# Optimization experiments

Measured on AMD Instinct MI355X. Metric: run time of the kernel, lower is better.

The kernel has to match this reference:

```python
import jax, jax.numpy as jnp
import numpy as np

B, K, DIN, D, NH, HD, FF = 16384, 64, 49, 16, 2, 8, 32
EPS = 1e-5


def _ln(x, g, b):
    m = jnp.mean(x, axis=-1, keepdims=True)
    v = jnp.mean((x - m) ** 2, axis=-1, keepdims=True)
    return (x - m) / jnp.sqrt(v + EPS) * g + b


def setup_inputs() -> dict:
    key = jax.random.key(0)
    ks = jax.random.split(key, 20)
    s = 0.05
    return {
        "x": jax.random.normal(ks[0], (B, K, DIN), dtype=jnp.float32),
        # torch Linear layout: weight is [out, in]
        "proj_w": jax.random.normal(ks[1], (D, DIN), dtype=jnp.float32) * s,
        "proj_b": jax.random.normal(ks[2], (D,), dtype=jnp.float32) * s,
        "pos": jax.random.normal(ks[3], (1, K, D), dtype=jnp.float32) * s,
        "in_proj_w": jax.random.normal(ks[4], (3 * D, D), dtype=jnp.float32) * s,
        "in_proj_b": jax.random.normal(ks[5], (3 * D,), dtype=jnp.float32) * s,
        "out_w": jax.random.normal(ks[6], (D, D), dtype=jnp.float32) * s,
        "out_b": jax.random.normal(ks[7], (D,), dtype=jnp.float32) * s,
        "ln1_g": jnp.ones((D,), dtype=jnp.float32),
        "ln1_b": jnp.zeros((D,), dtype=jnp.float32),
        "lin1_w": jax.random.normal(ks[8], (FF, D), dtype=jnp.float32) * s,
        "lin1_b": jax.random.normal(ks[9], (FF,), dtype=jnp.float32) * s,
        "lin2_w": jax.random.normal(ks[10], (D, FF), dtype=jnp.float32) * s,
        "lin2_b": jax.random.normal(ks[11], (D,), dtype=jnp.float32) * s,
        "ln2_g": jnp.ones((D,), dtype=jnp.float32),
        "ln2_b": jnp.zeros((D,), dtype=jnp.float32),
        "head_w": jax.random.normal(ks[12], (1, D), dtype=jnp.float32) * s,
        "head_b": jax.random.normal(ks[13], (1,), dtype=jnp.float32) * s,
    }


def reference(x, proj_w, proj_b, pos, in_proj_w, in_proj_b, out_w, out_b,
              ln1_g, ln1_b, lin1_w, lin1_b, lin2_w, lin2_b, ln2_g, ln2_b,
              head_w, head_b):
    # input projection + learned positional embedding
    h = jnp.einsum("bki,di->bkd", x, proj_w) + proj_b + pos  # [B,K,D]

    # --- self-attention (torch MultiheadAttention, post-norm encoder layer) ---
    qkv = jnp.einsum("bkd,ed->bke", h, in_proj_w) + in_proj_b  # [B,K,3D]
    q, k, v = jnp.split(qkv, 3, axis=-1)
    q = q.reshape(B, K, NH, HD)
    k = k.reshape(B, K, NH, HD)
    v = v.reshape(B, K, NH, HD)
    scores = jnp.einsum("bqhd,bkhd->bhqk", q, k) / jnp.sqrt(jnp.float32(HD))
    attn = jax.nn.softmax(scores, axis=-1)
    ctx = jnp.einsum("bhqk,bkhd->bqhd", attn, v).reshape(B, K, D)
    attn_out = jnp.einsum("bkd,od->bko", ctx, out_w) + out_b
    h = _ln(h + attn_out, ln1_g, ln1_b)

    # --- FFN (relu), post-norm ---
    ff = jnp.einsum("bkd,fd->bkf", h, lin1_w) + lin1_b
    ff = jax.nn.relu(ff)
    ff = jnp.einsum("bkf,df->bkd", ff, lin2_w) + lin2_b
    h = _ln(h + ff, ln2_g, ln2_b)

    # mean pool over sequence, then scalar head
    pooled = h.mean(axis=1)  # [B,D]
    out = jnp.einsum("bd,od->bo", pooled, head_w) + head_b
    return out.squeeze(-1)  # [B]
```

## Files before the change

### kernel.cpp

```cpp
#include <hip/hip_runtime.h>


#define SCALE 0.510069729f

#define KRS   24
#define VTB   1536
#define VTS   72
#define PRB   2688
#define PRS   72
#define HRB   7296
#define HRS   40
#define RED   9856
#define SMTOT 9864

#define WS_HB   2304
#define WS_EP   3328

typedef __bf16 v8bf __attribute__((ext_vector_type(8)));
typedef float  v4f  __attribute__((ext_vector_type(4)));

#define LDS_ORDER() __asm__ volatile("" ::: "memory")

static __device__ __forceinline__ short f2bs(float f) {
    __bf16 h = (__bf16)f;
    return __builtin_bit_cast(short, h);
}
#define MFMA(a,b,c) __builtin_amdgcn_mfma_f32_16x16x32_bf16((a),(b),(c),0,0,0)

template<int IMM> static __device__ __forceinline__ float swz(float x) {
    return __builtin_bit_cast(float,
        __builtin_amdgcn_ds_swizzle(__builtin_bit_cast(int, x), IMM));
}

static __device__ __forceinline__ void red16(v4f& v) {
    #pragma unroll
    for (int r = 0; r < 4; ++r) v[r] += swz<0x041F>(v[r]);
    #pragma unroll
    for (int r = 0; r < 4; ++r) v[r] += swz<0x081F>(v[r]);
    #pragma unroll
    for (int r = 0; r < 4; ++r) v[r] += swz<0x101F>(v[r]);
    #pragma unroll
    for (int r = 0; r < 4; ++r) v[r] += swz<0x201F>(v[r]);
}

__global__ __launch_bounds__(64)
void tx_prep(const float* __restrict__ proj_w, const float* __restrict__ proj_b,
             const float* __restrict__ pos,
             const float* __restrict__ in_proj_w, const float* __restrict__ in_proj_b,
             const float* __restrict__ out_w, const float* __restrict__ out_b,
             const float* __restrict__ ln1_g, const float* __restrict__ ln1_b,
             const float* __restrict__ lin1_w, const float* __restrict__ lin1_b,
             const float* __restrict__ lin2_w, const float* __restrict__ lin2_b,
             const float* __restrict__ ln2_g, const float* __restrict__ ln2_b,
             const float* __restrict__ head_w, float* __restrict__ ws)
{
    const int lane = threadIdx.x, g = lane >> 4, c = lane & 15;
    v8bf* wf = (v8bf*)ws;
    v8bf F;
    #pragma unroll
    for (int j = 0; j < 8; ++j) F[j] = (__bf16)proj_w[c*49 + g*8 + j];
    wf[0*64 + lane] = F;
    #pragma unroll
    for (int j = 0; j < 8; ++j) { int k = 32 + g*8 + j; F[j] = (k < 49) ? (__bf16)proj_w[c*49 + k] : (__bf16)0.f; }
    wf[1*64 + lane] = F;
    #pragma unroll
    for (int nt = 0; nt < 3; ++nt) {
        #pragma unroll
        for (int j = 0; j < 8; ++j) { int k = g*8 + j; F[j] = (k < 16) ? (__bf16)in_proj_w[(nt*16 + c)*16 + k] : (__bf16)0.f; }
        wf[(2 + nt)*64 + lane] = F;
    }
    #pragma unroll
    for (int j = 0; j < 8; ++j) { int k = g*8 + j; F[j] = (k < 16) ? (__bf16)out_w[c*16 + k] : (__bf16)0.f; }
    wf[5*64 + lane] = F;
    #pragma unroll
    for (int nt = 0; nt < 2; ++nt) {
        #pragma unroll
        for (int j = 0; j < 8; ++j) { int k = g*8 + j; F[j] = (k < 16) ? (__bf16)lin1_w[(nt*16 + c)*16 + k] : (__bf16)0.f; }
        wf[(6 + nt)*64 + lane] = F;
    }
    #pragma unroll
    for (int j = 0; j < 8; ++j) F[j] = (__bf16)lin2_w[c*32 + g*8 + j];
    wf[8*64 + lane] = F;

    float* hb = ws + WS_HB;
    #pragma unroll
    for (int ww = 0; ww < 4; ++ww)
        #pragma unroll
        for (int r = 0; r < 4; ++r)
            hb[ww*256 + lane*4 + r] = proj_b[c] + pos[(ww*16 + g*4 + r)*16 + c];

    if (lane < 16) {
        float* ep = ws + WS_EP + lane*16;
        ep[0]  = in_proj_b[lane];
        ep[1]  = in_proj_b[16 + lane] * SCALE;
        ep[2]  = in_proj_b[32 + lane];
        ep[3]  = out_b[lane];
        ep[4]  = ln1_g[lane];
        ep[5]  = ln1_b[lane];
        ep[6]  = lin1_b[lane];
        ep[7]  = lin1_b[16 + lane];
        ep[8]  = lin2_b[lane];
        ep[9]  = ln2_g[lane];
        ep[10] = ln2_b[lane];
        ep[11] = head_w[lane];
        ep[12] = 0.f; ep[13] = 0.f; ep[14] = 0.f; ep[15] = 0.f;
    }
}

__global__ __launch_bounds__(256, 8)
void tx_main(const float* __restrict__ x, const float* __restrict__ ws,
             const float* __restrict__ head_b, float* __restrict__ out)
{
    __shared__ __align__(16) short sm[SMTOT];
    const int tid   = threadIdx.x;
    const int w     = tid >> 6;
    const int lane  = tid & 63;
    const int g     = lane >> 4;
    const int c     = lane & 15;
    const int b     = blockIdx.x;
    const int myrow = w*16 + c;
    const int tok0  = w*16 + g*4;
    const v8bf* wf  = (const v8bf*)ws;
    const float4* ep4 = (const float4*)(ws + WS_EP);
    float* smf = (float*)sm;

    v8bf zfrag;
    #pragma unroll
    for (int j = 0; j < 8; ++j) zfrag[j] = (__bf16)0.f;
    const v4f zacc = {0.f, 0.f, 0.f, 0.f};

    const float4* xb4 = (const float4*)(x + (size_t)b * 3136);
    float4* sf4 = (float4*)smf;
    #pragma unroll
    for (int i = 0; i < 3; ++i) sf4[tid + i*256] = xb4[tid + i*256];
    if (tid < 16)      sf4[768 + tid] = xb4[768 + tid];
    else if (tid < 32) smf[3136 + tid - 16] = 0.f;
    *(unsigned long long*)&sm[HRB + myrow*HRS + 16 + g*4] = 0ull;
    __syncthreads();

    v4f hC;
    {
        const float* xr = smf + myrow*49 + g*8;
        v8bf a0, a1;
        #pragma unroll
        for (int j = 0; j < 8; ++j) a0[j] = (__bf16)xr[j];
        #pragma unroll
        for (int j = 0; j < 8; ++j) a1[j] = (__bf16)xr[32 + j];
        v8bf Bp0 = wf[0*64 + lane], Bp1 = wf[1*64 + lane];
        hC = MFMA(a0, Bp0, zacc);
        hC = MFMA(a1, Bp1, hC);
        v4f hb = ((const v4f*)(ws + WS_HB))[w*64 + lane];
        #pragma unroll
        for (int r = 0; r < 4; ++r) hC[r] += hb[r];
        #pragma unroll
        for (int r = 0; r < 4; ++r) sm[HRB + (tok0 + r)*HRS + c] = f2bs(hC[r]);
    }
    __syncthreads();

    {
        v8bf Bq0 = wf[2*64 + lane], Bq1 = wf[3*64 + lane], Bq2 = wf[4*64 + lane];
        v8bf a = *(const v8bf*)&sm[HRB + myrow*HRS + g*8];
        v4f qC = MFMA(a, Bq0, zacc);
        v4f kC = MFMA(a, Bq1, zacc);
        v4f vC = MFMA(a, Bq2, zacc);
        float4 e0 = ep4[c*4];
        #pragma unroll
        for (int r = 0; r < 4; ++r) {
            int tok = tok0 + r;
            sm[HRB + tok*HRS + c] = f2bs(qC[r] + e0.x);
            sm[tok*KRS + c]       = f2bs(fmaf(kC[r], SCALE, e0.y));
            sm[VTB + c*VTS + tok] = f2bs(vC[r] + e0.z);
        }
    }
    __syncthreads();

    v4f ctxC0, ctxC1;
    {
        v8bf aq = *(const v8bf*)&sm[HRB + myrow*HRS + g*8];
        const int ch  = c >> 3;
        const int pwb = PRB + tok0*PRS + (c & 7);
        const int prd = PRB + myrow*PRS + ((g ^ ((myrow >> 2) & 3)) << 3);
        #pragma unroll
        for (int hh = 0; hh < 2; ++hh) {
            v4f sC[4];
            #pragma unroll
            for (int tj = 0; tj < 4; ++tj) {
                v8bf bk = zfrag;
                if (g == hh) bk = *(const v8bf*)&sm[(tj*16 + c)*KRS + g*8];
                sC[tj] = MFMA(aq, bk, zacc);
            }
            #pragma unroll
            for (int tj = 0; tj < 4; ++tj) {
                int po = pwb + (((tj*2 + ch) ^ g) << 3);
                #pragma unroll
                for (int r = 0; r < 4; ++r)
                    sm[po + r*PRS] = f2bs(__builtin_amdgcn_exp2f(sC[tj][r]));
            }
            v8bf bv0 = zfrag, bv1 = zfrag;
            bool act  = (hh == 0) ? (c < 8) : (c >= 8);
            int  onec = (hh == 0) ? 8 : 7;
            if (act) {
                bv0 = *(const v8bf*)&sm[VTB + c*VTS + g*8];
                bv1 = *(const v8bf*)&sm[VTB + c*VTS + 32 + g*8];
            } else if (c == onec) {
                #pragma unroll
                for (int j = 0; j < 8; ++j) { bv0[j] = (__bf16)1.f; bv1[j] = (__bf16)1.f; }
            }
            LDS_ORDER();
            v4f acc = zacc;
            acc = MFMA(*(const v8bf*)&sm[prd],      bv0, acc);
            acc = MFMA(*(const v8bf*)&sm[prd + 32], bv1, acc);
            if (hh) ctxC1 = acc; else ctxC0 = acc;
            LDS_ORDER();
        }
    }

    {
        #pragma unroll
        for (int r = 0; r < 4; ++r) {
            float l0 = swz<0x110>(ctxC0[r]);
            float l1 = swz<0x0F0>(ctxC1[r]);
            float num = (c < 8) ? ctxC0[r] : ctxC1[r];
            float den = (c < 8) ? l0 : l1;
            sm[HRB + (tok0 + r)*HRS + c] = f2bs(num * __builtin_amdgcn_rcpf(den));
        }
    }
    LDS_ORDER();

    v4f hln;
    {
        v8bf Bo = wf[5*64 + lane];
        v8bf a = *(const v8bf*)&sm[HRB + myrow*HRS + g*8];
        v4f oC = MFMA(a, Bo, zacc);
        float4 e0 = ep4[c*4];
        float4 e1 = ep4[c*4 + 1];
        v4f hn, s, q;
        #pragma unroll
        for (int r = 0; r < 4; ++r) { hn[r] = hC[r] + oC[r] + e0.w; s[r] = hn[r]; q[r] = hn[r]*hn[r]; }
        red16(s);
        red16(q);
        #pragma unroll
        for (int r = 0; r < 4; ++r) {
            float mean = s[r]*0.0625f;
            float var  = fmaf(q[r], 0.0625f, -mean*mean);
            float is = __builtin_amdgcn_rsqf(var + 1e-5f);
            hln[r] = (hn[r] - mean)*is*e1.x + e1.y;
            sm[HRB + (tok0 + r)*HRS + c] = f2bs(hln[r]);
        }
    }
    LDS_ORDER();

    v4f o2;
    {
        v8bf Bl10 = wf[6*64 + lane], Bl11 = wf[7*64 + lane], Bl2 = wf[8*64 + lane];
        v8bf a = *(const v8bf*)&sm[HRB + myrow*HRS + g*8];
        v4f f0 = MFMA(a, Bl10, zacc);
        v4f f1 = MFMA(a, Bl11, zacc);
        float4 e1 = ep4[c*4 + 1];
        #pragma unroll
        for (int r = 0; r < 4; ++r) {
            int tok = tok0 + r;
            sm[HRB + tok*HRS + c]      = f2bs(fmaxf(f0[r] + e1.z, 0.f));
            sm[HRB + tok*HRS + 16 + c] = f2bs(fmaxf(f1[r] + e1.w, 0.f));
        }
        LDS_ORDER();
        v8bf a2 = *(const v8bf*)&sm[HRB + myrow*HRS + g*8];
        o2 = MFMA(a2, Bl2, zacc);
    }

    float part = 0.f;
    {
        float4 e2 = ep4[c*4 + 2];
        v4f hn, s, q;
        #pragma unroll
        for (int r = 0; r < 4; ++r) { hn[r] = hln[r] + o2[r] + e2.x; s[r] = hn[r]; q[r] = hn[r]*hn[r]; }
        red16(s);
        red16(q);
        #pragma unroll
        for (int r = 0; r < 4; ++r) {
            float mean = s[r]*0.0625f;
            float var  = fmaf(q[r], 0.0625f, -mean*mean);
            float is = __builtin_amdgcn_rsqf(var + 1e-5f);
            float h3 = (hn[r] - mean)*is*e2.y + e2.z;
            part = fmaf(h3, e2.w, part);
        }
    }
    part += swz<0x041F>(part);
    part += swz<0x081F>(part);
    part += swz<0x101F>(part);
    part += swz<0x201F>(part);
    part += swz<0x401F>(part);
    part += __shfl_xor(part, 32, 64);
    float* fred = (float*)&sm[RED];
    if (lane == 0) fred[w] = part;
    __syncthreads();
    if (tid == 0)
        out[b] = (fred[0] + fred[1] + fred[2] + fred[3]) * (1.f/64.f) + head_b[0];
}

extern "C" void kernel_launch(void* const* d_in, const int* in_sizes, int n_in,
                              void* d_out, int out_size, void* d_ws, size_t ws_size,
                              hipStream_t stream) {
    const float* x         = (const float*)d_in[0];
    const float* proj_w    = (const float*)d_in[1];
    const float* proj_b    = (const float*)d_in[2];
    const float* pos       = (const float*)d_in[3];
    const float* in_proj_w = (const float*)d_in[4];
    const float* in_proj_b = (const float*)d_in[5];
    const float* out_w     = (const float*)d_in[6];
    const float* out_b     = (const float*)d_in[7];
    const float* ln1_g     = (const float*)d_in[8];
    const float* ln1_b     = (const float*)d_in[9];
    const float* lin1_w    = (const float*)d_in[10];
    const float* lin1_b    = (const float*)d_in[11];
    const float* lin2_w    = (const float*)d_in[12];
    const float* lin2_b    = (const float*)d_in[13];
    const float* ln2_g     = (const float*)d_in[14];
    const float* ln2_b     = (const float*)d_in[15];
    const float* head_w    = (const float*)d_in[16];
    const float* head_b    = (const float*)d_in[17];
    float* ws = (float*)d_ws;

    tx_prep<<<1, 64, 0, stream>>>(proj_w, proj_b, pos, in_proj_w, in_proj_b,
                                  out_w, out_b, ln1_g, ln1_b, lin1_w, lin1_b,
                                  lin2_w, lin2_b, ln2_g, ln2_b, head_w, ws);
    tx_main<<<16384, 256, 0, stream>>>(x, ws, head_b, (float*)d_out);
}
```

Before: 332.8 us.

## Keep attention probabilities in registers via transposed score MFMA

```diff
diff --git a/kernel.cpp b/kernel.cpp
--- a/kernel.cpp
+++ b/kernel.cpp
@@ -6,12 +6,10 @@
 #define KRS   24
 #define VTB   1536
 #define VTS   72
-#define PRB   2688
-#define PRS   72
-#define HRB   7296
+#define HRB   6304
 #define HRS   40
-#define RED   9856
-#define SMTOT 9864
+#define RED   8864
+#define SMTOT 8872
 
 #define WS_HB   2304
 #define WS_EP   3328
@@ -146,30 +144,31 @@
         for (int j = 0; j < 8; ++j) a0[j] = (__bf16)xr[j];
         #pragma unroll
         for (int j = 0; j < 8; ++j) a1[j] = (__bf16)xr[32 + j];
-        v8bf Bp0 = wf[0*64 + lane], Bp1 = wf[1*64 + lane];
-        hC = MFMA(a0, Bp0, zacc);
-        hC = MFMA(a1, Bp1, hC);
         v4f hb = ((const v4f*)(ws + WS_HB))[w*64 + lane];
-        #pragma unroll
-        for (int r = 0; r < 4; ++r) hC[r] += hb[r];
+        hC = MFMA(a0, wf[0*64 + lane], hb);
+        hC = MFMA(a1, wf[1*64 + lane], hC);
         #pragma unroll
         for (int r = 0; r < 4; ++r) sm[HRB + (tok0 + r)*HRS + c] = f2bs(hC[r]);
     }
     __syncthreads();
 
     {
-        v8bf Bq0 = wf[2*64 + lane], Bq1 = wf[3*64 + lane], Bq2 = wf[4*64 + lane];
+        if (tid < 64) {
+            float4 z4 = {0.f, 0.f, 0.f, 0.f};
+            *(float4*)&sm[tid*KRS + 16] = z4;
+        }
         v8bf a = *(const v8bf*)&sm[HRB + myrow*HRS + g*8];
-        v4f qC = MFMA(a, Bq0, zacc);
-        v4f kC = MFMA(a, Bq1, zacc);
-        v4f vC = MFMA(a, Bq2, zacc);
+        v4f qC = MFMA(a, wf[2*64 + lane], zacc);
+        v4f kC = MFMA(a, wf[3*64 + lane], zacc);
+        v4f vC = MFMA(a, wf[4*64 + lane], zacc);
         float4 e0 = ep4[c*4];
+        const int vsl = VTB + c*VTS + 32*(w >> 1) + 8*g + 4*(w & 1);
         #pragma unroll
         for (int r = 0; r < 4; ++r) {
             int tok = tok0 + r;
             sm[HRB + tok*HRS + c] = f2bs(qC[r] + e0.x);
             sm[tok*KRS + c]       = f2bs(fmaf(kC[r], SCALE, e0.y));
-            sm[VTB + c*VTS + tok] = f2bs(vC[r] + e0.z);
+            sm[vsl + r]           = f2bs(vC[r] + e0.z);
         }
     }
     __syncthreads();
@@ -177,24 +176,29 @@
     v4f ctxC0, ctxC1;
     {
         v8bf aq = *(const v8bf*)&sm[HRB + myrow*HRS + g*8];
-        const int ch  = c >> 3;
-        const int pwb = PRB + tok0*PRS + (c & 7);
-        const int prd = PRB + myrow*PRS + ((g ^ ((myrow >> 2) & 3)) << 3);
         #pragma unroll
         for (int hh = 0; hh < 2; ++hh) {
-            v4f sC[4];
-            #pragma unroll
-            for (int tj = 0; tj < 4; ++tj) {
-                v8bf bk = zfrag;
-                if (g == hh) bk = *(const v8bf*)&sm[(tj*16 + c)*KRS + g*8];
-                sC[tj] = MFMA(aq, bk, zacc);
-            }
-            #pragma unroll
-            for (int tj = 0; tj < 4; ++tj) {
-                int po = pwb + (((tj*2 + ch) ^ g) << 3);
+            v8bf bq = (g == hh) ? aq : zfrag;
+            v8bf plo, phi;
+            {
+                v8bf ak0 = *(const v8bf*)&sm[(0*16 + c)*KRS + g*8];
+                v8bf ak1 = *(const v8bf*)&sm[(1*16 + c)*KRS + g*8];
+                v4f s0 = MFMA(ak0, bq, zacc);
+                v4f s1 = MFMA(ak1, bq, zacc);
                 #pragma unroll
-                for (int r = 0; r < 4; ++r)
-                    sm[po + r*PRS] = f2bs(__builtin_amdgcn_exp2f(sC[tj][r]));
+                for (int r = 0; r < 4; ++r) {
+                    plo[r]     = (__bf16)__builtin_amdgcn_exp2f(s0[r]);
+                    plo[4 + r] = (__bf16)__builtin_amdgcn_exp2f(s1[r]);
+                }
+                v8bf ak2 = *(const v8bf*)&sm[(2*16 + c)*KRS + g*8];
+                v8bf ak3 = *(const v8bf*)&sm[(3*16 + c)*KRS + g*8];
+                v4f s2 = MFMA(ak2, bq, zacc);
+                v4f s3 = MFMA(ak3, bq, zacc);
+                #pragma unroll
+                for (int r = 0; r < 4; ++r) {
+                    phi[r]     = (__bf16)__builtin_amdgcn_exp2f(s2[r]);
+                    phi[4 + r] = (__bf16)__builtin_amdgcn_exp2f(s3[r]);
+                }
             }
             v8bf bv0 = zfrag, bv1 = zfrag;
             bool act  = (hh == 0) ? (c < 8) : (c >= 8);
@@ -206,12 +210,9 @@
                 #pragma unroll
                 for (int j = 0; j < 8; ++j) { bv0[j] = (__bf16)1.f; bv1[j] = (__bf16)1.f; }
             }
-            LDS_ORDER();
-            v4f acc = zacc;
-            acc = MFMA(*(const v8bf*)&sm[prd],      bv0, acc);
-            acc = MFMA(*(const v8bf*)&sm[prd + 32], bv1, acc);
+            v4f acc = MFMA(plo, bv0, zacc);
+            acc = MFMA(phi, bv1, acc);
             if (hh) ctxC1 = acc; else ctxC0 = acc;
-            LDS_ORDER();
         }
     }
 
@@ -229,14 +230,13 @@
 
     v4f hln;
     {
-        v8bf Bo = wf[5*64 + lane];
         v8bf a = *(const v8bf*)&sm[HRB + myrow*HRS + g*8];
-        v4f oC = MFMA(a, Bo, zacc);
+        v4f oC = MFMA(a, wf[5*64 + lane], hC);
         float4 e0 = ep4[c*4];
         float4 e1 = ep4[c*4 + 1];
         v4f hn, s, q;
         #pragma unroll
-        for (int r = 0; r < 4; ++r) { hn[r] = hC[r] + oC[r] + e0.w; s[r] = hn[r]; q[r] = hn[r]*hn[r]; }
+        for (int r = 0; r < 4; ++r) { hn[r] = oC[r] + e0.w; s[r] = hn[r]; q[r] = hn[r]*hn[r]; }
         red16(s);
         red16(q);
         #pragma unroll
@@ -252,10 +252,9 @@
 
     v4f o2;
     {
-        v8bf Bl10 = wf[6*64 + lane], Bl11 = wf[7*64 + lane], Bl2 = wf[8*64 + lane];
         v8bf a = *(const v8bf*)&sm[HRB + myrow*HRS + g*8];
-        v4f f0 = MFMA(a, Bl10, zacc);
-        v4f f1 = MFMA(a, Bl11, zacc);
+        v4f f0 = MFMA(a, wf[6*64 + lane], zacc);
+        v4f f1 = MFMA(a, wf[7*64 + lane], zacc);
         float4 e1 = ep4[c*4 + 1];
         #pragma unroll
         for (int r = 0; r < 4; ++r) {
@@ -265,7 +264,7 @@
         }
         LDS_ORDER();
         v8bf a2 = *(const v8bf*)&sm[HRB + myrow*HRS + g*8];
-        o2 = MFMA(a2, Bl2, zacc);
+        o2 = MFMA(a2, wf[8*64 + lane], hln);
     }
 
     float part = 0.f;
@@ -273,7 +272,7 @@
         float4 e2 = ep4[c*4 + 2];
         v4f hn, s, q;
         #pragma unroll
-        for (int r = 0; r < 4; ++r) { hn[r] = hln[r] + o2[r] + e2.x; s[r] = hn[r]; q[r] = hn[r]*hn[r]; }
+        for (int r = 0; r < 4; ++r) { hn[r] = o2[r] + e2.x; s[r] = hn[r]; q[r] = hn[r]*hn[r]; }
         red16(s);
         red16(q);
         #pragma unroll
```

Result: no change. 327.9 us (-1.5%).
